# Performance work log

Measured on AMD Instinct MI355X. Metric: run time of the kernel, lower is better.

The kernel has to match this reference:

```python
import jax, jax.numpy as jnp
import numpy as np

B, S, D = 8, 1024, 256


def _linear_params(key, d):
    k1, k2 = jax.random.split(key)
    lim = 1.0 / np.sqrt(d)
    W = jax.random.uniform(k1, (d, d), jnp.float32, -lim, lim)
    b = jax.random.uniform(k2, (d,), jnp.float32, -lim, lim)
    return W, b


def setup_inputs() -> dict:
    key = jax.random.key(0)
    ks = jax.random.split(key, 7)
    x = jax.random.normal(ks[0], (B, S, D), jnp.float32)
    Wq, bq = _linear_params(ks[1], D)
    Wk, bk = _linear_params(ks[2], D)
    Wv, bv = _linear_params(ks[3], D)
    Wf, bf = _linear_params(ks[4], D)
    Wi, bi = _linear_params(ks[5], D)
    Wo, bo = _linear_params(ks[6], D)
    return {"x": x, "Wq": Wq, "bq": bq, "Wk": Wk, "bk": bk, "Wv": Wv, "bv": bv,
            "Wf": Wf, "bf": bf, "Wi": Wi, "bi": bi, "Wo": Wo, "bo": bo}


def reference(x, Wq, bq, Wk, bk, Wv, bv, Wf, bf, Wi, bi, Wo, bo):
    # Projections (torch Linear stores W as [out, in])
    q = x @ Wq.T + bq
    k = x @ Wk.T + bk
    v = x @ Wq.T + bq  # faithful to source: forward uses self.W_q(x) for v (W_v unused)
    f = jax.nn.sigmoid(x @ Wf.T + bf)  # forget gate, sigmoid
    i = jnp.exp(x @ Wi.T + bi)         # input gate, exp

    # time-major xs: each (S, B, D)
    xs = tuple(jnp.swapaxes(a, 0, 1) for a in (f, i, k, v, q))
    C0 = jnp.zeros((x.shape[0], x.shape[2], x.shape[2]), x.dtype)  # matrix memory [B,D,D]
    n0 = jnp.zeros((x.shape[0], x.shape[2]), x.dtype)              # normalizer [B,D]

    def step(carry, t):
        C, n = carry
        ft, it, kt, vt, qt = t
        # C_t = f_t * C_{t-1} + i_t * v_t k_t^T  (gates broadcast over key dim)
        C = ft[:, :, None] * C + it[:, :, None] * (vt[:, :, None] * kt[:, None, :])
        n = ft * n + it * kt
        num = jnp.einsum('bik,bk->bi', C, qt)
        den = jnp.maximum(jnp.abs(jnp.einsum('bk,bk->b', n, qt)), 1.0)[:, None]
        return (C, n), num / den

    _, h = jax.lax.scan(step, (C0, n0), xs)
    h = jnp.swapaxes(h, 0, 1)  # (B, S, D)
    return h @ Wo.T + bo
```

## Files before the change

kernel.cpp:

```cpp
#include <hip/hip_runtime.h>
#include <math.h>

namespace {

constexpr int Bn = 8;
constexpr int Sn = 1024;
constexpr int Dn = 256;
constexpr int Mn = Bn * Sn;
constexpr int L  = 32;
constexpr int NSEG = Sn / L;

typedef __attribute__((ext_vector_type(8))) short short8;
typedef __attribute__((ext_vector_type(4))) float f32x4;

__device__ float g_den[Bn * Sn];

__device__ __forceinline__ float sigmoidf_(float x) {
    return 1.0f / (1.0f + __expf(-x));
}

__device__ __forceinline__ unsigned short f2bf(float x) {
    unsigned int u = __float_as_uint(x);
    return (unsigned short)((u + 0x7FFF + ((u >> 16) & 1)) >> 16);
}
__device__ __forceinline__ float bf2f(unsigned short h) {
    return __uint_as_float(((unsigned int)h) << 16);
}

__device__ __forceinline__ void multi_reduce16(float v[16], int lane) {
    {   const bool hi = (lane & 32) != 0;
        #pragma unroll
        for (int i = 0; i < 8; ++i) {
            const float send = hi ? v[i] : v[i + 8];
            const float recv = __shfl_xor(send, 32, 64);
            v[i] = (hi ? v[i + 8] : v[i]) + recv;
        } }
    {   const bool hi = (lane & 16) != 0;
        #pragma unroll
        for (int i = 0; i < 4; ++i) {
            const float send = hi ? v[i] : v[i + 4];
            const float recv = __shfl_xor(send, 16, 64);
            v[i] = (hi ? v[i + 4] : v[i]) + recv;
        } }
    {   const bool hi = (lane & 8) != 0;
        #pragma unroll
        for (int i = 0; i < 2; ++i) {
            const float send = hi ? v[i] : v[i + 2];
            const float recv = __shfl_xor(send, 8, 64);
            v[i] = (hi ? v[i + 2] : v[i]) + recv;
        } }
    {   const bool hi = (lane & 4) != 0;
        const float send = hi ? v[0] : v[1];
        const float recv = __shfl_xor(send, 4, 64);
        v[0] = (hi ? v[1] : v[0]) + recv;
    }
    v[0] += __shfl_xor(v[0], 2, 64);
    v[0] += __shfl_xor(v[0], 1, 64);
}

__global__ __launch_bounds__(256) void proj_gemm(
    const float* __restrict__ X,
    const float* __restrict__ W0, const float* __restrict__ b0,
    const float* __restrict__ W1, const float* __restrict__ b1,
    const float* __restrict__ W2, const float* __restrict__ b2,
    const float* __restrict__ W3, const float* __restrict__ b3,
    float* __restrict__ Y0, float* __restrict__ Y1,
    float* __restrict__ Y2, float* __restrict__ Y3)
{
    __shared__ unsigned short Ah[128][40];
    __shared__ unsigned short Al[128][40];
    __shared__ unsigned short Bh[128][40];
    __shared__ unsigned short Bl[128][40];

    const int tid = threadIdx.x;
    const int mb  = blockIdx.x * 128;
    const int nbg = blockIdx.y;
    const int widx = nbg >> 1;
    const int ro   = (nbg & 1) * 128;

    const float* Wsel = (widx == 0) ? W0 : (widx == 1) ? W1 : (widx == 2) ? W2 : W3;
    const float* bsel = (widx == 0) ? b0 : (widx == 1) ? b1 : (widx == 2) ? b2 : b3;
    float*       Ysel = (widx == 0) ? Y0 : (widx == 1) ? Y1 : (widx == 2) ? Y2 : Y3;

    const int lane = tid & 63;
    const int wv   = tid >> 6;
    const int wm   = (wv >> 1) * 64;
    const int wn   = (wv & 1) * 64;
    const int quad = lane >> 4;
    const int l16  = lane & 15;
    const int srow = tid >> 1;
    const int skq  = (tid & 1) * 16;

    f32x4 acc[4][4];
    #pragma unroll
    for (int mt = 0; mt < 4; ++mt)
        #pragma unroll
        for (int nt = 0; nt < 4; ++nt)
            acc[mt][nt] = (f32x4){0.f, 0.f, 0.f, 0.f};

    for (int k0 = 0; k0 < Dn; k0 += 32) {
        float4 xa[4], wb[4];
        #pragma unroll
        for (int c = 0; c < 4; ++c) {
            xa[c] = *(const float4*)(X    + (size_t)(mb + srow) * Dn + k0 + skq + 4 * c);
            wb[c] = *(const float4*)(Wsel + (size_t)(ro + srow) * Dn + k0 + skq + 4 * c);
        }
        __syncthreads();
        #pragma unroll
        for (int c = 0; c < 4; ++c) {
            const float xs[4] = {xa[c].x, xa[c].y, xa[c].z, xa[c].w};
            const float wsv[4] = {wb[c].x, wb[c].y, wb[c].z, wb[c].w};
            ushort4 h, l;
            unsigned short t0;
            t0 = f2bf(xs[0]); h.x = t0; l.x = f2bf(xs[0] - bf2f(t0));
            t0 = f2bf(xs[1]); h.y = t0; l.y = f2bf(xs[1] - bf2f(t0));
            t0 = f2bf(xs[2]); h.z = t0; l.z = f2bf(xs[2] - bf2f(t0));
            t0 = f2bf(xs[3]); h.w = t0; l.w = f2bf(xs[3] - bf2f(t0));
            *(ushort4*)&Ah[srow][skq + 4 * c] = h;
            *(ushort4*)&Al[srow][skq + 4 * c] = l;
            t0 = f2bf(wsv[0]); h.x = t0; l.x = f2bf(wsv[0] - bf2f(t0));
            t0 = f2bf(wsv[1]); h.y = t0; l.y = f2bf(wsv[1] - bf2f(t0));
            t0 = f2bf(wsv[2]); h.z = t0; l.z = f2bf(wsv[2] - bf2f(t0));
            t0 = f2bf(wsv[3]); h.w = t0; l.w = f2bf(wsv[3] - bf2f(t0));
            *(ushort4*)&Bh[srow][skq + 4 * c] = h;
            *(ushort4*)&Bl[srow][skq + 4 * c] = l;
        }
        __syncthreads();

        short8 afh[4], afl[4];
        #pragma unroll
        for (int mt = 0; mt < 4; ++mt) {
            const int row = wm + mt * 16 + l16;
            afh[mt] = *(const short8*)&Ah[row][quad * 8];
            afl[mt] = *(const short8*)&Al[row][quad * 8];
        }
        #pragma unroll
        for (int nt = 0; nt < 4; ++nt) {
            const int row = wn + nt * 16 + l16;
            const short8 bfh = *(const short8*)&Bh[row][quad * 8];
            const short8 bfl = *(const short8*)&Bl[row][quad * 8];
            #pragma unroll
            for (int mt = 0; mt < 4; ++mt) {
                acc[mt][nt] = __builtin_amdgcn_mfma_f32_16x16x32_bf16(
                    afh[mt], bfh, acc[mt][nt], 0, 0, 0);
                acc[mt][nt] = __builtin_amdgcn_mfma_f32_16x16x32_bf16(
                    afh[mt], bfl, acc[mt][nt], 0, 0, 0);
                acc[mt][nt] = __builtin_amdgcn_mfma_f32_16x16x32_bf16(
                    afl[mt], bfh, acc[mt][nt], 0, 0, 0);
            }
        }
    }

    #pragma unroll
    for (int nt = 0; nt < 4; ++nt) {
        const int col = ro + wn + nt * 16 + l16;
        const float bv = bsel[col];
        #pragma unroll
        for (int mt = 0; mt < 4; ++mt) {
            const int rowb = mb + wm + mt * 16 + quad * 4;
            #pragma unroll
            for (int r = 0; r < 4; ++r) {
                float v = acc[mt][nt][r] + bv;
                if (widx == 2)      v = sigmoidf_(v);
                else if (widx == 3) v = __expf(v);
                Ysel[(size_t)(rowb + r) * Dn + col] = v;
            }
        }
    }
}

__global__ __launch_bounds__(256) void out_gemm(
    const float* __restrict__ X, const float* __restrict__ W,
    const float* __restrict__ bias, float* __restrict__ Y)
{
    __shared__ unsigned short Ah[128][40];
    __shared__ unsigned short Al[128][40];
    __shared__ unsigned short Bh[128][40];
    __shared__ unsigned short Bl[128][40];

    const int tid = threadIdx.x;
    const int mb  = blockIdx.x * 128;
    const int nb  = blockIdx.y * 128;

    const int lane = tid & 63;
    const int wv   = tid >> 6;
    const int wm   = (wv >> 1) * 64;
    const int wn   = (wv & 1) * 64;
    const int quad = lane >> 4;
    const int l16  = lane & 15;
    const int srow = tid >> 1;
    const int skq  = (tid & 1) * 16;

    const float invd = 1.0f / fmaxf(fabsf(g_den[mb + srow]), 1.0f);

    f32x4 acc[4][4];
    #pragma unroll
    for (int mt = 0; mt < 4; ++mt)
        #pragma unroll
        for (int nt = 0; nt < 4; ++nt)
            acc[mt][nt] = (f32x4){0.f, 0.f, 0.f, 0.f};

    for (int k0 = 0; k0 < Dn; k0 += 32) {
        float4 xa[4], wb[4];
        #pragma unroll
        for (int c = 0; c < 4; ++c) {
            xa[c] = *(const float4*)(X + (size_t)(mb + srow) * Dn + k0 + skq + 4 * c);
            wb[c] = *(const float4*)(W + (size_t)(nb + srow) * Dn + k0 + skq + 4 * c);
            xa[c].x *= invd; xa[c].y *= invd; xa[c].z *= invd; xa[c].w *= invd;
        }
        __syncthreads();
        #pragma unroll
        for (int c = 0; c < 4; ++c) {
            const float xs[4] = {xa[c].x, xa[c].y, xa[c].z, xa[c].w};
            const float wsv[4] = {wb[c].x, wb[c].y, wb[c].z, wb[c].w};
            ushort4 h, l;
            unsigned short t0;
            t0 = f2bf(xs[0]); h.x = t0; l.x = f2bf(xs[0] - bf2f(t0));
            t0 = f2bf(xs[1]); h.y = t0; l.y = f2bf(xs[1] - bf2f(t0));
            t0 = f2bf(xs[2]); h.z = t0; l.z = f2bf(xs[2] - bf2f(t0));
            t0 = f2bf(xs[3]); h.w = t0; l.w = f2bf(xs[3] - bf2f(t0));
            *(ushort4*)&Ah[srow][skq + 4 * c] = h;
            *(ushort4*)&Al[srow][skq + 4 * c] = l;
            t0 = f2bf(wsv[0]); h.x = t0; l.x = f2bf(wsv[0] - bf2f(t0));
            t0 = f2bf(wsv[1]); h.y = t0; l.y = f2bf(wsv[1] - bf2f(t0));
            t0 = f2bf(wsv[2]); h.z = t0; l.z = f2bf(wsv[2] - bf2f(t0));
            t0 = f2bf(wsv[3]); h.w = t0; l.w = f2bf(wsv[3] - bf2f(t0));
            *(ushort4*)&Bh[srow][skq + 4 * c] = h;
            *(ushort4*)&Bl[srow][skq + 4 * c] = l;
        }
        __syncthreads();

        short8 afh[4], afl[4];
        #pragma unroll
        for (int mt = 0; mt < 4; ++mt) {
            const int row = wm + mt * 16 + l16;
            afh[mt] = *(const short8*)&Ah[row][quad * 8];
            afl[mt] = *(const short8*)&Al[row][quad * 8];
        }
        #pragma unroll
        for (int nt = 0; nt < 4; ++nt) {
            const int row = wn + nt * 16 + l16;
            const short8 bfh = *(const short8*)&Bh[row][quad * 8];
            const short8 bfl = *(const short8*)&Bl[row][quad * 8];
            #pragma unroll
            for (int mt = 0; mt < 4; ++mt) {
                acc[mt][nt] = __builtin_amdgcn_mfma_f32_16x16x32_bf16(
                    afh[mt], bfh, acc[mt][nt], 0, 0, 0);
                acc[mt][nt] = __builtin_amdgcn_mfma_f32_16x16x32_bf16(
                    afh[mt], bfl, acc[mt][nt], 0, 0, 0);
                acc[mt][nt] = __builtin_amdgcn_mfma_f32_16x16x32_bf16(
                    afl[mt], bfh, acc[mt][nt], 0, 0, 0);
            }
        }
    }

    #pragma unroll
    for (int nt = 0; nt < 4; ++nt) {
        const int col = nb + wn + nt * 16 + l16;
        const float bv = bias[col];
        #pragma unroll
        for (int mt = 0; mt < 4; ++mt) {
            const int rowb = mb + wm + mt * 16 + quad * 4;
            #pragma unroll
            for (int r = 0; r < 4; ++r) {
                Y[(size_t)(rowb + r) * Dn + col] = acc[mt][nt][r] + bv;
            }
        }
    }
}

__global__ __launch_bounds__(256) void gate_prep(
    const float* __restrict__ Pf, const float* __restrict__ Pi,
    const float* __restrict__ Pk, const float* __restrict__ Pq,
    float* __restrict__ Gc, float* __restrict__ Vt, float* __restrict__ Nt,
    float* __restrict__ Aend, float* __restrict__ un)
{
    const int m = blockIdx.x;
    const int b = blockIdx.y;
    const int r = threadIdx.x;
    const size_t base = (size_t)b * Sn * Dn + (size_t)m * L * Dn + r;

    float G = 1.0f, Nacc = 0.0f;
    #pragma unroll 4
    for (int t = 0; t < L; ++t) {
        const size_t off = base + (size_t)t * Dn;
        const float f  = Pf[off];
        const float iv = Pi[off];
        const float kv = Pk[off];
        const float vv = Pq[off];
        G *= f;
        const float rG = 1.0f / G;
        Gc[off] = G;
        Vt[off] = iv * vv * rG;
        Nacc = fmaf(iv * kv, rG, Nacc);
        Nt[off] = Nacc;
    }
    const size_t s = ((size_t)b * NSEG + m) * Dn + r;
    Aend[s] = G;
    un[s]   = G * Nacc;
}

__global__ __launch_bounds__(256) void ut_gemm(
    const float* __restrict__ Pk, const float* __restrict__ Vt,
    const float* __restrict__ Aend, float* __restrict__ UT)
{
    __shared__ float As[L][68];
    __shared__ float Bs[L][68];

    const int bm   = blockIdx.x;
    const int tile = blockIdx.y;
    const int cb   = (tile >> 2) * 64;
    const int rb   = (tile & 3) * 64;
    const int b    = bm >> 5;
    const int m    = bm & 31;
    const size_t kb = (size_t)b * Sn * Dn + (size_t)m * L * Dn;
    const int tid = threadIdx.x;

    #pragma unroll
    for (int n = 0; n < 8; ++n) {
        const int e  = n * 256 + tid;
        const int sg = e >> 6;
        const int cc = e & 63;
        As[sg][cc] = Pk[kb + (size_t)sg * Dn + cb + cc];
        Bs[sg][cc] = Vt[kb + (size_t)sg * Dn + rb + cc];
    }
    __syncthreads();

    const int tx = tid & 15;
    const int ty = tid >> 4;
    float acc[4][4];
    #pragma unroll
    for (int i = 0; i < 4; ++i)
        #pragma unroll
        for (int j = 0; j < 4; ++j) acc[i][j] = 0.0f;

    #pragma unroll
    for (int sg = 0; sg < L; ++sg) {
        const float4 a4 = *(const float4*)&As[sg][ty * 4];
        const float4 b4 = *(const float4*)&Bs[sg][tx * 4];
        const float aa[4] = {a4.x, a4.y, a4.z, a4.w};
        const float bb[4] = {b4.x, b4.y, b4.z, b4.w};
        #pragma unroll
        for (int i = 0; i < 4; ++i)
            #pragma unroll
            for (int j = 0; j < 4; ++j)
                acc[i][j] = fmaf(aa[i], bb[j], acc[i][j]);
    }

    const float4 g4 = *(const float4*)(Aend + (size_t)bm * Dn + rb + tx * 4);
    float* ub = UT + (size_t)bm * Dn * Dn;
    #pragma unroll
    for (int i = 0; i < 4; ++i) {
        float4 o;
        o.x = acc[i][0] * g4.x; o.y = acc[i][1] * g4.y;
        o.z = acc[i][2] * g4.z; o.w = acc[i][3] * g4.w;
        *(float4*)(ub + (size_t)(cb + ty * 4 + i) * Dn + rb + tx * 4) = o;
    }
}

__global__ __launch_bounds__(256) void compose(
    const float* __restrict__ UT, const float* __restrict__ Aend,
    const float* __restrict__ un,
    float* __restrict__ CinT, float* __restrict__ nin)
{
    const int gx = blockIdx.x;
    const int b  = blockIdx.y;
    const int tid = threadIdx.x;

    if (gx == 64) {
        const int r = tid;
        float acc = 0.0f;
        for (int m = 0; m < NSEG; ++m) {
            const size_t s = ((size_t)b * NSEG + m) * Dn + r;
            nin[s] = acc;
            acc = fmaf(Aend[s], acc, un[s]);
        }
        return;
    }

    const int id = gx * 256 + tid;
    const int c  = id >> 6;
    const int r4 = (id & 63) * 4;

    float4 acc = make_float4(0.f, 0.f, 0.f, 0.f);
    for (int m = 0; m < NSEG; ++m) {
        const size_t bm  = (size_t)b * NSEG + m;
        const size_t idx = bm * Dn * Dn + (size_t)c * Dn + r4;
        *(float4*)(CinT + idx) = acc;
        const float4 a4 = *(const float4*)(Aend + bm * Dn + r4);
        const float4 u4 = *(const float4*)(UT + idx);
        acc.x = fmaf(a4.x, acc.x, u4.x);
        acc.y = fmaf(a4.y, acc.y, u4.y);
        acc.z = fmaf(a4.z, acc.z, u4.z);
        acc.w = fmaf(a4.w, acc.w, u4.w);
    }
}

__global__ __launch_bounds__(256) void s_gemm(
    const float* __restrict__ Pk, const float* __restrict__ Pq,
    float* __restrict__ Ssm)
{
    const int m = blockIdx.x;
    const int b = blockIdx.y;
    const size_t qb = (size_t)b * Sn * Dn + (size_t)m * L * Dn;
    const int tid = threadIdx.x;
    const int tau = tid >> 3;
    const int s4  = (tid & 7) * 4;

    float a0 = 0.f, a1 = 0.f, a2 = 0.f, a3 = 0.f;
    #pragma unroll 4
    for (int c = 0; c < Dn; c += 4) {
        const float4 q4 = *(const float4*)(Pq + qb + (size_t)tau * Dn + c);
        const float4 k0 = *(const float4*)(Pk + qb + (size_t)(s4 + 0) * Dn + c);
        const float4 k1 = *(const float4*)(Pk + qb + (size_t)(s4 + 1) * Dn + c);
        const float4 k2 = *(const float4*)(Pk + qb + (size_t)(s4 + 2) * Dn + c);
        const float4 k3 = *(const float4*)(Pk + qb + (size_t)(s4 + 3) * Dn + c);
        a0 += q4.x*k0.x + q4.y*k0.y + q4.z*k0.z + q4.w*k0.w;
        a1 += q4.x*k1.x + q4.y*k1.y + q4.z*k1.z + q4.w*k1.w;
        a2 += q4.x*k2.x + q4.y*k2.y + q4.z*k2.z + q4.w*k2.w;
        a3 += q4.x*k3.x + q4.y*k3.y + q4.z*k3.z + q4.w*k3.w;
    }
    float* out = Ssm + ((size_t)b * NSEG + m) * L * L + (size_t)tau * L + s4;
    out[0] = (s4 + 0 <= tau) ? a0 : 0.0f;
    out[1] = (s4 + 1 <= tau) ? a1 : 0.0f;
    out[2] = (s4 + 2 <= tau) ? a2 : 0.0f;
    out[3] = (s4 + 3 <= tau) ? a3 : 0.0f;
}

__global__ __launch_bounds__(256) void num_gemm(
    const float* __restrict__ Pq, const float* __restrict__ Vt,
    const float* __restrict__ Gc, const float* __restrict__ Ssm,
    const float* __restrict__ CinT, float* __restrict__ Pnum)
{
    __shared__ float Sld[L][33];
    __shared__ float Qld[L][257];

    const int rb = blockIdx.x * 128;
    const int m  = blockIdx.y;
    const int b  = blockIdx.z;
    const size_t qb = (size_t)b * Sn * Dn + (size_t)m * L * Dn;
    const size_t ub = ((size_t)b * NSEG + m) * Dn * Dn;
    const size_t sb = ((size_t)b * NSEG + m) * L * L;
    const int tid = threadIdx.x;

    #pragma unroll
    for (int n = 0; n < 4; ++n) {
        const int e = n * 256 + tid;
        Sld[e >> 5][e & 31] = Ssm[sb + e];
    }
    #pragma unroll
    for (int n = 0; n < L; ++n)
        Qld[n][tid] = Pq[qb + (size_t)n * Dn + tid];
    __syncthreads();

    const int tx = tid & 31;
    const int ty = tid >> 5;
    const int r4 = rb + tx * 4;
    const int t4 = ty * 4;

    float4 acc[4];
    #pragma unroll
    for (int i = 0; i < 4; ++i) acc[i] = make_float4(0.f, 0.f, 0.f, 0.f);

    #pragma unroll 4
    for (int sg = 0; sg < L; ++sg) {
        const float4 v4 = *(const float4*)(Vt + qb + (size_t)sg * Dn + r4);
        #pragma unroll
        for (int i = 0; i < 4; ++i) {
            const float s = Sld[t4 + i][sg];
            acc[i].x = fmaf(s, v4.x, acc[i].x);
            acc[i].y = fmaf(s, v4.y, acc[i].y);
            acc[i].z = fmaf(s, v4.z, acc[i].z);
            acc[i].w = fmaf(s, v4.w, acc[i].w);
        }
    }

    #pragma unroll 8
    for (int c = 0; c < Dn; ++c) {
        const float4 ct = *(const float4*)(CinT + ub + (size_t)c * Dn + r4);
        #pragma unroll
        for (int i = 0; i < 4; ++i) {
            const float q = Qld[t4 + i][c];
            acc[i].x = fmaf(q, ct.x, acc[i].x);
            acc[i].y = fmaf(q, ct.y, acc[i].y);
            acc[i].z = fmaf(q, ct.z, acc[i].z);
            acc[i].w = fmaf(q, ct.w, acc[i].w);
        }
    }

    #pragma unroll
    for (int i = 0; i < 4; ++i) {
        const size_t off = qb + (size_t)(t4 + i) * Dn + r4;
        const float4 g4 = *(const float4*)(Gc + off);
        float4 o;
        o.x = acc[i].x * g4.x; o.y = acc[i].y * g4.y;
        o.z = acc[i].z * g4.z; o.w = acc[i].w * g4.w;
        *(float4*)(Pnum + off) = o;
    }
}

__global__ __launch_bounds__(256) void den_kernel(
    const float* __restrict__ Pq, const float* __restrict__ Gc,
    const float* __restrict__ Nt, const float* __restrict__ nin)
{
    const int gx = blockIdx.x;
    const int b  = blockIdx.y;
    const int tid  = threadIdx.x;
    const int lane = tid & 63;
    const int wv   = tid >> 6;
    const int c4   = lane * 4;

    const int tbase = gx * 64 + wv * 16;
    float p[16];
    #pragma unroll
    for (int j = 0; j < 16; ++j) {
        const int t = tbase + j;
        const int m = t >> 5;
        const size_t off = (size_t)b * Sn * Dn + (size_t)t * Dn + c4;
        const float4 q4 = *(const float4*)(Pq + off);
        const float4 g4 = *(const float4*)(Gc + off);
        const float4 n4 = *(const float4*)(Nt + off);
        const float4 i4 = *(const float4*)(nin + ((size_t)b * NSEG + m) * Dn + c4);
        p[j] = q4.x * g4.x * (i4.x + n4.x)
             + q4.y * g4.y * (i4.y + n4.y)
             + q4.z * g4.z * (i4.z + n4.z)
             + q4.w * g4.w * (i4.w + n4.w);
    }
    multi_reduce16(p, lane);
    if ((lane & 3) == 0)
        g_den[b * Sn + tbase + ((lane >> 2) & 15)] = p[0];
}

}

extern "C" void kernel_launch(void* const* d_in, const int* in_sizes, int n_in,
                              void* d_out, int out_size, void* d_ws, size_t ws_size,
                              hipStream_t stream)
{
    const float* x  = (const float*)d_in[0];
    const float* Wq = (const float*)d_in[1];  const float* bq = (const float*)d_in[2];
    const float* Wk = (const float*)d_in[3];  const float* bk = (const float*)d_in[4];
    const float* Wf = (const float*)d_in[7];  const float* bf = (const float*)d_in[8];
    const float* Wi = (const float*)d_in[9];  const float* bi = (const float*)d_in[10];
    const float* Wo = (const float*)d_in[11]; const float* bo = (const float*)d_in[12];
    float* out = (float*)d_out;

    float* ws = (float*)d_ws;
    const size_t sz = (size_t)Mn * Dn;
    float* Pq = ws;
    float* Pk = ws + sz;
    float* Pf = ws + 2 * sz;
    float* Pi = ws + 3 * sz;
    float* Pn = ws + 4 * sz;
    float* Gc = ws + 5 * sz;
    float* Vt = ws + 6 * sz;
    float* Nt = ws + 7 * sz;
    float* UT   = ws + 8 * sz;
    float* CinT = ws + 16 * sz;
    float* Ssm  = ws + 24 * sz;
    float* Aend = Ssm + (size_t)Bn * NSEG * L * L;
    float* un   = Aend + (size_t)Bn * NSEG * Dn;
    float* nin  = un   + (size_t)Bn * NSEG * Dn;

    proj_gemm<<<dim3(Mn / 128, 8), 256, 0, stream>>>(
        x, Wq, bq, Wk, bk, Wf, bf, Wi, bi, Pq, Pk, Pf, Pi);

    gate_prep<<<dim3(NSEG, Bn), 256, 0, stream>>>(
        Pf, Pi, Pk, Pq, Gc, Vt, Nt, Aend, un);

    ut_gemm<<<dim3(Bn * NSEG, 16), 256, 0, stream>>>(Pk, Vt, Aend, UT);

    compose<<<dim3(65, Bn), 256, 0, stream>>>(UT, Aend, un, CinT, nin);

    s_gemm<<<dim3(NSEG, Bn), 256, 0, stream>>>(Pk, Pq, Ssm);

    num_gemm<<<dim3(2, NSEG, Bn), 256, 0, stream>>>(
        Pq, Vt, Gc, Ssm, CinT, Pn);

    den_kernel<<<dim3(16, Bn), 256, 0, stream>>>(Pq, Gc, Nt, nin);

    out_gemm<<<dim3(Mn / 128, Dn / 128), 256, 0, stream>>>(Pn, Wo, bo, out);
}
```

Measured before the change: 234.3 us.

## Fuse s_gemm into gate prep and denominator into num_gemm with atomics

The intra-chunk q·k score computation moves into the gate-prep kernel, and the denominator reduction moves into the epilogue of num_gemm using shuffle reductions and atomicAdd into g_den, which prep zeroes first. This removes two kernel launches and the separate pass that re-read Pq, Gc and Nt for the denominator. In exchange, prep does more serial work per block, num_gemm loads more data per thread, and the atomic accumulation makes the floating-point summation order nondeterministic.

```diff
diff --git a/kernel.cpp b/kernel.cpp
--- a/kernel.cpp
+++ b/kernel.cpp
@@ -25,37 +25,6 @@
 }
 __device__ __forceinline__ float bf2f(unsigned short h) {
     return __uint_as_float(((unsigned int)h) << 16);
-}
-
-__device__ __forceinline__ void multi_reduce16(float v[16], int lane) {
-    {   const bool hi = (lane & 32) != 0;
-        #pragma unroll
-        for (int i = 0; i < 8; ++i) {
-            const float send = hi ? v[i] : v[i + 8];
-            const float recv = __shfl_xor(send, 32, 64);
-            v[i] = (hi ? v[i + 8] : v[i]) + recv;
-        } }
-    {   const bool hi = (lane & 16) != 0;
-        #pragma unroll
-        for (int i = 0; i < 4; ++i) {
-            const float send = hi ? v[i] : v[i + 4];
-            const float recv = __shfl_xor(send, 16, 64);
-            v[i] = (hi ? v[i + 4] : v[i]) + recv;
-        } }
-    {   const bool hi = (lane & 8) != 0;
-        #pragma unroll
-        for (int i = 0; i < 2; ++i) {
-            const float send = hi ? v[i] : v[i + 2];
-            const float recv = __shfl_xor(send, 8, 64);
-            v[i] = (hi ? v[i + 2] : v[i]) + recv;
-        } }
-    {   const bool hi = (lane & 4) != 0;
-        const float send = hi ? v[0] : v[1];
-        const float recv = __shfl_xor(send, 4, 64);
-        v[0] = (hi ? v[1] : v[0]) + recv;
-    }
-    v[0] += __shfl_xor(v[0], 2, 64);
-    v[0] += __shfl_xor(v[0], 1, 64);
 }
 
 __global__ __launch_bounds__(256) void proj_gemm(
@@ -269,35 +238,65 @@
     }
 }
 
-__global__ __launch_bounds__(256) void gate_prep(
+__global__ __launch_bounds__(256) void prep(
     const float* __restrict__ Pf, const float* __restrict__ Pi,
     const float* __restrict__ Pk, const float* __restrict__ Pq,
     float* __restrict__ Gc, float* __restrict__ Vt, float* __restrict__ Nt,
-    float* __restrict__ Aend, float* __restrict__ un)
+    float* __restrict__ Aend, float* __restrict__ un, float* __restrict__ Ssm)
 {
     const int m = blockIdx.x;
     const int b = blockIdx.y;
-    const int r = threadIdx.x;
-    const size_t base = (size_t)b * Sn * Dn + (size_t)m * L * Dn + r;
-
-    float G = 1.0f, Nacc = 0.0f;
-    #pragma unroll 4
-    for (int t = 0; t < L; ++t) {
-        const size_t off = base + (size_t)t * Dn;
-        const float f  = Pf[off];
-        const float iv = Pi[off];
-        const float kv = Pk[off];
-        const float vv = Pq[off];
-        G *= f;
-        const float rG = 1.0f / G;
-        Gc[off] = G;
-        Vt[off] = iv * vv * rG;
-        Nacc = fmaf(iv * kv, rG, Nacc);
-        Nt[off] = Nacc;
-    }
-    const size_t s = ((size_t)b * NSEG + m) * Dn + r;
-    Aend[s] = G;
-    un[s]   = G * Nacc;
+    const int tid = threadIdx.x;
+
+    if (tid < L) g_den[b * Sn + m * L + tid] = 0.0f;
+
+    {
+        const int r = tid;
+        const size_t base = (size_t)b * Sn * Dn + (size_t)m * L * Dn + r;
+        float G = 1.0f, Nacc = 0.0f;
+        #pragma unroll 4
+        for (int t = 0; t < L; ++t) {
+            const size_t off = base + (size_t)t * Dn;
+            const float f  = Pf[off];
+            const float iv = Pi[off];
+            const float kv = Pk[off];
+            const float vv = Pq[off];
+            G *= f;
+            const float rG = 1.0f / G;
+            Gc[off] = G;
+            Vt[off] = iv * vv * rG;
+            Nacc = fmaf(iv * kv, rG, Nacc);
+            Nt[off] = Nacc;
+        }
+        const size_t s = ((size_t)b * NSEG + m) * Dn + r;
+        Aend[s] = G;
+        un[s]   = G * Nacc;
+    }
+
+    {
+        const size_t qb = (size_t)b * Sn * Dn + (size_t)m * L * Dn;
+        const int tau = tid >> 3;
+        const int s4  = (tid & 7) * 4;
+
+        float a0 = 0.f, a1 = 0.f, a2 = 0.f, a3 = 0.f;
+        #pragma unroll 4
+        for (int c = 0; c < Dn; c += 4) {
+            const float4 q4 = *(const float4*)(Pq + qb + (size_t)tau * Dn + c);
+            const float4 k0 = *(const float4*)(Pk + qb + (size_t)(s4 + 0) * Dn + c);
+            const float4 k1 = *(const float4*)(Pk + qb + (size_t)(s4 + 1) * Dn + c);
+            const float4 k2 = *(const float4*)(Pk + qb + (size_t)(s4 + 2) * Dn + c);
+            const float4 k3 = *(const float4*)(Pk + qb + (size_t)(s4 + 3) * Dn + c);
+            a0 += q4.x*k0.x + q4.y*k0.y + q4.z*k0.z + q4.w*k0.w;
+            a1 += q4.x*k1.x + q4.y*k1.y + q4.z*k1.z + q4.w*k1.w;
+            a2 += q4.x*k2.x + q4.y*k2.y + q4.z*k2.z + q4.w*k2.w;
+            a3 += q4.x*k3.x + q4.y*k3.y + q4.z*k3.z + q4.w*k3.w;
+        }
+        float* outp = Ssm + ((size_t)b * NSEG + m) * L * L + (size_t)tau * L + s4;
+        outp[0] = (s4 + 0 <= tau) ? a0 : 0.0f;
+        outp[1] = (s4 + 1 <= tau) ? a1 : 0.0f;
+        outp[2] = (s4 + 2 <= tau) ? a2 : 0.0f;
+        outp[3] = (s4 + 3 <= tau) ? a3 : 0.0f;
+    }
 }
 
 __global__ __launch_bounds__(256) void ut_gemm(
@@ -396,41 +395,11 @@
     }
 }
 
-__global__ __launch_bounds__(256) void s_gemm(
-    const float* __restrict__ Pk, const float* __restrict__ Pq,
-    float* __restrict__ Ssm)
-{
-    const int m = blockIdx.x;
-    const int b = blockIdx.y;
-    const size_t qb = (size_t)b * Sn * Dn + (size_t)m * L * Dn;
-    const int tid = threadIdx.x;
-    const int tau = tid >> 3;
-    const int s4  = (tid & 7) * 4;
-
-    float a0 = 0.f, a1 = 0.f, a2 = 0.f, a3 = 0.f;
-    #pragma unroll 4
-    for (int c = 0; c < Dn; c += 4) {
-        const float4 q4 = *(const float4*)(Pq + qb + (size_t)tau * Dn + c);
-        const float4 k0 = *(const float4*)(Pk + qb + (size_t)(s4 + 0) * Dn + c);
-        const float4 k1 = *(const float4*)(Pk + qb + (size_t)(s4 + 1) * Dn + c);
-        const float4 k2 = *(const float4*)(Pk + qb + (size_t)(s4 + 2) * Dn + c);
-        const float4 k3 = *(const float4*)(Pk + qb + (size_t)(s4 + 3) * Dn + c);
-        a0 += q4.x*k0.x + q4.y*k0.y + q4.z*k0.z + q4.w*k0.w;
-        a1 += q4.x*k1.x + q4.y*k1.y + q4.z*k1.z + q4.w*k1.w;
-        a2 += q4.x*k2.x + q4.y*k2.y + q4.z*k2.z + q4.w*k2.w;
-        a3 += q4.x*k3.x + q4.y*k3.y + q4.z*k3.z + q4.w*k3.w;
-    }
-    float* out = Ssm + ((size_t)b * NSEG + m) * L * L + (size_t)tau * L + s4;
-    out[0] = (s4 + 0 <= tau) ? a0 : 0.0f;
-    out[1] = (s4 + 1 <= tau) ? a1 : 0.0f;
-    out[2] = (s4 + 2 <= tau) ? a2 : 0.0f;
-    out[3] = (s4 + 3 <= tau) ? a3 : 0.0f;
-}
-
 __global__ __launch_bounds__(256) void num_gemm(
     const float* __restrict__ Pq, const float* __restrict__ Vt,
     const float* __restrict__ Gc, const float* __restrict__ Ssm,
-    const float* __restrict__ CinT, float* __restrict__ Pnum)
+    const float* __restrict__ CinT, const float* __restrict__ Nt,
+    const float* __restrict__ nin, float* __restrict__ Pnum)
 {
     __shared__ float Sld[L][33];
     __shared__ float Qld[L][257];
@@ -488,47 +457,35 @@
         }
     }
 
+    const float4 i4 = *(const float4*)(nin + ((size_t)b * NSEG + m) * Dn + r4);
+    float dp[4];
     #pragma unroll
     for (int i = 0; i < 4; ++i) {
         const size_t off = qb + (size_t)(t4 + i) * Dn + r4;
         const float4 g4 = *(const float4*)(Gc + off);
+        const float4 q4 = *(const float4*)(Pq + off);
+        const float4 n4 = *(const float4*)(Nt + off);
         float4 o;
         o.x = acc[i].x * g4.x; o.y = acc[i].y * g4.y;
         o.z = acc[i].z * g4.z; o.w = acc[i].w * g4.w;
         *(float4*)(Pnum + off) = o;
-    }
-}
-
-__global__ __launch_bounds__(256) void den_kernel(
-    const float* __restrict__ Pq, const float* __restrict__ Gc,
-    const float* __restrict__ Nt, const float* __restrict__ nin)
-{
-    const int gx = blockIdx.x;
-    const int b  = blockIdx.y;
-    const int tid  = threadIdx.x;
-    const int lane = tid & 63;
-    const int wv   = tid >> 6;
-    const int c4   = lane * 4;
-
-    const int tbase = gx * 64 + wv * 16;
-    float p[16];
-    #pragma unroll
-    for (int j = 0; j < 16; ++j) {
-        const int t = tbase + j;
-        const int m = t >> 5;
-        const size_t off = (size_t)b * Sn * Dn + (size_t)t * Dn + c4;
-        const float4 q4 = *(const float4*)(Pq + off);
-        const float4 g4 = *(const float4*)(Gc + off);
-        const float4 n4 = *(const float4*)(Nt + off);
-        const float4 i4 = *(const float4*)(nin + ((size_t)b * NSEG + m) * Dn + c4);
-        p[j] = q4.x * g4.x * (i4.x + n4.x)
-             + q4.y * g4.y * (i4.y + n4.y)
-             + q4.z * g4.z * (i4.z + n4.z)
-             + q4.w * g4.w * (i4.w + n4.w);
-    }
-    multi_reduce16(p, lane);
-    if ((lane & 3) == 0)
-        g_den[b * Sn + tbase + ((lane >> 2) & 15)] = p[0];
+        dp[i] = q4.x * g4.x * (i4.x + n4.x)
+              + q4.y * g4.y * (i4.y + n4.y)
+              + q4.z * g4.z * (i4.z + n4.z)
+              + q4.w * g4.w * (i4.w + n4.w);
+    }
+
+    #pragma unroll
+    for (int s = 1; s < 32; s <<= 1) {
+        #pragma unroll
+        for (int i = 0; i < 4; ++i)
+            dp[i] += __shfl_xor(dp[i], s, 64);
+    }
+    if (tx == 0) {
+        #pragma unroll
+        for (int i = 0; i < 4; ++i)
+            atomicAdd(&g_den[b * Sn + m * L + t4 + i], dp[i]);
+    }
 }
 
 }
@@ -565,19 +522,15 @@
     proj_gemm<<<dim3(Mn / 128, 8), 256, 0, stream>>>(
         x, Wq, bq, Wk, bk, Wf, bf, Wi, bi, Pq, Pk, Pf, Pi);
 
-    gate_prep<<<dim3(NSEG, Bn), 256, 0, stream>>>(
-        Pf, Pi, Pk, Pq, Gc, Vt, Nt, Aend, un);
+    prep<<<dim3(NSEG, Bn), 256, 0, stream>>>(
+        Pf, Pi, Pk, Pq, Gc, Vt, Nt, Aend, un, Ssm);
 
     ut_gemm<<<dim3(Bn * NSEG, 16), 256, 0, stream>>>(Pk, Vt, Aend, UT);
 
     compose<<<dim3(65, Bn), 256, 0, stream>>>(UT, Aend, un, CinT, nin);
 
-    s_gemm<<<dim3(NSEG, Bn), 256, 0, stream>>>(Pk, Pq, Ssm);
-
     num_gemm<<<dim3(2, NSEG, Bn), 256, 0, stream>>>(
-        Pq, Vt, Gc, Ssm, CinT, Pn);
-
-    den_kernel<<<dim3(16, Bn), 256, 0, stream>>>(Pq, Gc, Nt, nin);
+        Pq, Vt, Gc, Ssm, CinT, Nt, nin, Pn);
 
     out_gemm<<<dim3(Mn / 128, Dn / 128), 256, 0, stream>>>(Pn, Wo, bo, out);
 }
```

After: 231.2 us. About the same (-1.3%).
